# Kernel tuning notes

Measured on AMD Instinct MI355X. Metric: run time of the kernel, lower is better.

## Reference

```python
import jax, jax.numpy as jnp
import numpy as np

N = 10000    # nodes
D = 128      # d_model
K = 16       # d_state
S = 5        # seq_len (tokens per node)
E = 320000   # edges
R = 200      # num relation types
P = E // (S - 1)  # edges sampled per tokenizer step
EPS = 1e-5


def setup_inputs() -> dict:
    key = jax.random.key(0)
    ks = jax.random.split(key, 16)
    sc = 1.0 / np.sqrt(D)
    return {
        "x": jax.random.normal(ks[0], (N, D), jnp.float32),
        "edge_index": jax.random.randint(ks[1], (2, E), 0, N),
        "edge_type": jax.random.randint(ks[2], (E,), 0, R),
        "perms": jax.random.randint(ks[3], (S - 1, P), 0, E),
        "rel_table": jax.random.normal(ks[4], (R, D), jnp.float32) * 0.1,
        "log_A": jax.random.normal(ks[5], (D, K), jnp.float32) * 0.1,
        "W_B": jax.random.normal(ks[6], (D, K), jnp.float32) * sc,
        "W_C": jax.random.normal(ks[7], (D, K), jnp.float32) * sc,
        "W_delta": jax.random.normal(ks[8], (D, D), jnp.float32) * sc,
        "b_delta": jnp.zeros((D,), jnp.float32),
        "W_g": jax.random.normal(ks[9], (D, D), jnp.float32) * sc,
        "b_g": jnp.zeros((D,), jnp.float32),
        "W_out": jax.random.normal(ks[10], (D, D), jnp.float32) * sc,
        "b_out": jnp.zeros((D,), jnp.float32),
        "ln_g": jnp.ones((D,), jnp.float32),
        "ln_b": jnp.zeros((D,), jnp.float32),
    }


def _tokenize(x, edge_index, edge_type, perms, rel_table):
    # x: [N,D]; perms: [S-1,P] -> tokens [N,S,D]
    src, dst = edge_index[0], edge_index[1]
    step_src = src[perms]                    # [S-1,P]
    step_dst = dst[perms]                    # [S-1,P]
    msg = x[step_src] + rel_table[edge_type[perms]]  # [S-1,P,D]
    seg = jax.vmap(lambda i, m: jax.ops.segment_sum(m, i, num_segments=N))(step_dst, msg)  # [S-1,N,D]
    deg = jax.vmap(lambda i: jax.ops.segment_sum(jnp.ones((P,), x.dtype), i, num_segments=N))(step_dst)  # [S-1,N]
    neigh = seg / jnp.clip(deg, 1.0)[..., None]
    return jnp.concatenate([x[:, None, :], jnp.moveaxis(neigh, 0, 1)], axis=1)  # [N,S,D]


def _selective_scan(tokens, log_A, W_B, W_C, W_delta, b_delta):
    # tokens: [N,S,D] -> [N,S,D]
    deltas = jax.nn.softplus(tokens @ W_delta + b_delta)  # [N,S,D]
    Bs = tokens @ W_B                                     # [N,S,K]
    Cs = tokens @ W_C                                     # [N,S,K]
    A_cont = -jnp.exp(log_A)                              # [D,K]
    A_disc = jnp.exp(deltas[..., None] * A_cont)          # [N,S,D,K]
    Bx = deltas[..., None] * Bs[:, :, None, :] * tokens[..., None]  # [N,S,D,K] = B_disc * x_k

    def step(state, xs):
        a, bx, c = xs                          # [N,D,K],[N,D,K],[N,K]
        state = a * state + bx
        y = jnp.einsum('ndk,nk->nd', state, c)
        return state, y

    init = jnp.zeros((tokens.shape[0], D, K), tokens.dtype)
    _, ys = jax.lax.scan(step, init, (jnp.moveaxis(A_disc, 1, 0),
                                      jnp.moveaxis(Bx, 1, 0),
                                      jnp.moveaxis(Cs, 1, 0)))
    return jnp.moveaxis(ys, 0, 1)  # [N,S,D]


def reference(x, edge_index, edge_type, perms, rel_table, log_A, W_B, W_C,
              W_delta, b_delta, W_g, b_g, W_out, b_out, ln_g, ln_b):
    tokens = _tokenize(x, edge_index, edge_type, perms, rel_table)
    out_f = _selective_scan(tokens, log_A, W_B, W_C, W_delta, b_delta)
    out_b = _selective_scan(tokens[:, ::-1, :], log_A, W_B, W_C, W_delta, b_delta)
    scan_out = (out_f + out_b[:, ::-1, :]).mean(axis=1)  # [N,D]
    gate = jax.nn.silu(x @ W_g + b_g)
    res = x + gate * (scan_out @ W_out + b_out)
    mu = res.mean(axis=-1, keepdims=True)
    var = res.var(axis=-1, keepdims=True)
    return (res - mu) / jnp.sqrt(var + EPS) * ln_g + ln_b
```

## Files before the change

### kernel.cpp

```cpp
#include <hip/hip_runtime.h>
#include <hip/hip_bf16.h>
#include <math.h>

#define N_NODES 10000
#define D_MODEL 128
#define E_EDGES 320000
#define P_EDGES 80000
#define LN_EPS 1e-5f
#define CAP 32
#define M_ROWS 50000
#define NCOLS 160

typedef __attribute__((ext_vector_type(8))) short bf16x8;
typedef __attribute__((ext_vector_type(4))) float f32x4;

__device__ __forceinline__ unsigned short f2bf(float f) {
    __hip_bfloat16 h = __float2bfloat16(f);
    return *reinterpret_cast<unsigned short*>(&h);
}
__device__ __forceinline__ float bf2f(unsigned int u) {
    return __uint_as_float(u << 16);
}

__global__ __launch_bounds__(256) void prep_all(
    const float* __restrict__ Wd, const float* __restrict__ Wb,
    const float* __restrict__ Wc, const float* __restrict__ Wg,
    const float* __restrict__ W_out,
    const float* __restrict__ x, const float* __restrict__ rel,
    const int* __restrict__ edge_index, const int* __restrict__ edge_type,
    unsigned short* __restrict__ Bp, unsigned short* __restrict__ Wop,
    unsigned short* __restrict__ Wgp,
    unsigned short* __restrict__ x_bf, unsigned short* __restrict__ rel_bf,
    int* __restrict__ cnt, int4* __restrict__ ed4,
    unsigned short* __restrict__ tokens)
{
    int gid = blockIdx.x * 256 + threadIdx.x;
    if (gid < 20480) {
        int k = gid / NCOLS, n = gid - (gid / NCOLS) * NCOLS;
        float v;
        if (n < 128)      v = Wd[k * 128 + n];
        else if (n < 144) v = Wb[k * 16 + (n - 128)];
        else              v = Wc[k * 16 + (n - 144)];
        Bp[((size_t)(k >> 3) * NCOLS + n) * 8 + (k & 7)] = f2bf(v);
    } else if (gid < 36864) {
        int i = gid - 20480;
        int k = i >> 7, n = i & 127;
        Wop[((size_t)(k >> 3) * 128 + n) * 8 + (k & 7)] = f2bf(W_out[k * 128 + n]);
    } else if (gid < 53248) {
        int i = gid - 36864;
        int k = i >> 7, n = i & 127;
        Wgp[((size_t)(k >> 3) * 128 + n) * 8 + (k & 7)] = f2bf(Wg[k * 128 + n]);
    } else if (gid < 94208) {
        cnt[gid - 53248] = 0;
    } else if (gid < 119808) {
        int i = gid - 94208;
        rel_bf[i] = f2bf(rel[i]);
    } else if (gid < 1399808) {
        int i = gid - 119808;
        unsigned short v = f2bf(x[i]);
        x_bf[i] = v;
        tokens[(size_t)(i >> 7) * 640 + (i & 127)] = v;
    } else if (gid < 1719808) {
        int e = gid - 1399808;
        ed4[e] = make_int4(edge_index[e], edge_index[E_EDGES + e], edge_type[e], 0);
    }
}

__global__ __launch_bounds__(256) void csr_build(
    const int4* __restrict__ ed4, const int* __restrict__ perms,
    int* __restrict__ cnt, int2* __restrict__ slots)
{
    int gid = blockIdx.x * blockDim.x + threadIdx.x;
    if (gid >= 4 * P_EDGES) return;
    int s = gid / P_EDGES;
    int e = perms[gid];
    int4 ed = ed4[e];
    int b = ed.y * 4 + s;
    int pos = atomicAdd(&cnt[b], 1);
    if (pos < CAP) slots[(size_t)b * CAP + pos] = make_int2(ed.x, ed.z);
}

__global__ __launch_bounds__(256) void gather_tokens(
    const unsigned short* __restrict__ x_bf,
    const int* __restrict__ cnt, const int2* __restrict__ slots,
    const unsigned short* __restrict__ rel_bf,
    unsigned short* __restrict__ tokens)
{
    int n = blockIdx.x;
    int w = threadIdx.x >> 6, lane = threadIdx.x & 63;
    int b = n * 4 + w;
    int c = cnt[b];
    int cc = c < CAP ? c : CAP;
    const int2* sl = slots + (size_t)b * CAP;
    const unsigned int* xu = (const unsigned int*)x_bf;
    const unsigned int* ru = (const unsigned int*)rel_bf;
    float ax = 0.f, ay = 0.f;
    int j = 0;
    for (; j + 4 <= cc; j += 4) {
        int4 e01 = *(const int4*)(sl + j);
        int4 e23 = *(const int4*)(sl + j + 2);
        unsigned int x0 = xu[(size_t)e01.x * 64 + lane];
        unsigned int r0 = ru[(size_t)e01.y * 64 + lane];
        unsigned int x1 = xu[(size_t)e01.z * 64 + lane];
        unsigned int r1 = ru[(size_t)e01.w * 64 + lane];
        unsigned int x2 = xu[(size_t)e23.x * 64 + lane];
        unsigned int r2 = ru[(size_t)e23.y * 64 + lane];
        unsigned int x3 = xu[(size_t)e23.z * 64 + lane];
        unsigned int r3 = ru[(size_t)e23.w * 64 + lane];
        ax += (bf2f(x0 & 0xffffu) + bf2f(r0 & 0xffffu))
            + (bf2f(x1 & 0xffffu) + bf2f(r1 & 0xffffu))
            + (bf2f(x2 & 0xffffu) + bf2f(r2 & 0xffffu))
            + (bf2f(x3 & 0xffffu) + bf2f(r3 & 0xffffu));
        ay += (bf2f(x0 >> 16) + bf2f(r0 >> 16))
            + (bf2f(x1 >> 16) + bf2f(r1 >> 16))
            + (bf2f(x2 >> 16) + bf2f(r2 >> 16))
            + (bf2f(x3 >> 16) + bf2f(r3 >> 16));
    }
    if (j + 2 <= cc) {
        int4 e01 = *(const int4*)(sl + j);
        unsigned int x0 = xu[(size_t)e01.x * 64 + lane];
        unsigned int r0 = ru[(size_t)e01.y * 64 + lane];
        unsigned int x1 = xu[(size_t)e01.z * 64 + lane];
        unsigned int r1 = ru[(size_t)e01.w * 64 + lane];
        ax += (bf2f(x0 & 0xffffu) + bf2f(r0 & 0xffffu))
            + (bf2f(x1 & 0xffffu) + bf2f(r1 & 0xffffu));
        ay += (bf2f(x0 >> 16) + bf2f(r0 >> 16))
            + (bf2f(x1 >> 16) + bf2f(r1 >> 16));
        j += 2;
    }
    if (j < cc) {
        int2 se = sl[j];
        unsigned int xa = xu[(size_t)se.x * 64 + lane];
        unsigned int ra = ru[(size_t)se.y * 64 + lane];
        ax += bf2f(xa & 0xffffu) + bf2f(ra & 0xffffu);
        ay += bf2f(xa >> 16) + bf2f(ra >> 16);
    }
    float inv = 1.f / fmaxf((float)c, 1.f);
    unsigned int pack = (unsigned int)f2bf(ax * inv)
                      | ((unsigned int)f2bf(ay * inv) << 16);
    ((unsigned int*)tokens)[((size_t)n * 5 + w + 1) * 64 + lane] = pack;
}

__global__ __launch_bounds__(256, 2) void mega(
    const unsigned short* __restrict__ tokens,
    const unsigned short* __restrict__ Bp,
    const unsigned short* __restrict__ Wop,
    const unsigned short* __restrict__ Wgp,
    const unsigned short* __restrict__ x_bf,
    const float* __restrict__ x,
    const float* __restrict__ log_A,
    const float* __restrict__ b_delta, const float* __restrict__ b_g,
    const float* __restrict__ b_out,
    const float* __restrict__ ln_g, const float* __restrict__ ln_b,
    float* __restrict__ out)
{
    const int tid = threadIdx.x;
    const int wv = tid >> 6, lane = tid & 63;
    const int quad = lane >> 4, l16 = lane & 15;
    const int m0 = blockIdx.x * 80;
    const int n0 = blockIdx.x * 16;

    __shared__ __align__(16) char smem[34816];
    unsigned short* s_delta = (unsigned short*)smem;
    float*          s_bcf   = (float*)(smem + 20480);
    unsigned short* s_so    = (unsigned short*)(smem + 30720);
    float* s_res  = (float*)smem;
    float* s_pmu  = (float*)(smem + 20480);
    float* s_pv2  = (float*)(smem + 21504);
    float* s_mu   = (float*)(smem + 22528);
    float* s_rstd = (float*)(smem + 22592);

    for (int u = wv; u < 50; u += 4) {
        int f = u / 10, t = u - (u / 10) * 10;
        f32x4 acc = {0.f, 0.f, 0.f, 0.f};
        const unsigned short* arow =
            tokens + (size_t)(m0 + f * 16 + l16) * 128 + quad * 8;
        #pragma unroll
        for (int kc = 0; kc < 128; kc += 32) {
            bf16x8 a = *(const bf16x8*)(arow + kc);
            bf16x8 b = *(const bf16x8*)(Bp +
                ((size_t)(kc / 8 + quad) * NCOLS + 16 * t + l16) * 8);
            acc = __builtin_amdgcn_mfma_f32_16x16x32_bf16(a, b, acc, 0, 0, 0);
        }
        int rbase = f * 16 + quad * 4;
        int c = 16 * t + l16;
        #pragma unroll
        for (int reg = 0; reg < 4; ++reg) {
            int r = rbase + reg;
            float v = acc[reg];
            if (t < 8) {
                float z = v + b_delta[c];
                float d = (z > 15.f) ? z : log1pf(__expf(z));
                s_delta[r * 128 + c] = f2bf(d);
            } else {
                s_bcf[r * 32 + (c - 128)] = v;
            }
        }
    }
    __syncthreads();

    {
        const int dim = tid & 127;
        float Ac[16];
        {
            const float4* la = (const float4*)(log_A + dim * 16);
            #pragma unroll
            for (int q = 0; q < 4; ++q) {
                float4 lv = la[q];
                Ac[q * 4 + 0] = -__expf(lv.x);
                Ac[q * 4 + 1] = -__expf(lv.y);
                Ac[q * 4 + 2] = -__expf(lv.z);
                Ac[q * 4 + 3] = -__expf(lv.w);
            }
        }
        #pragma unroll 1
        for (int i = 0; i < 8; ++i) {
            int node = (tid >> 7) + 2 * i;
            const float* bcn = s_bcf + node * 160;
            float tv[5], dl[5];
            {
                const unsigned short* tb =
                    tokens + ((size_t)(n0 + node) * 5) * 128 + dim;
                const unsigned short* db = s_delta + node * 640 + dim;
                #pragma unroll
                for (int s = 0; s < 5; ++s) {
                    tv[s] = bf2f(tb[s * 128]);
                    dl[s] = bf2f(db[s * 128]);
                }
            }
            float st[16], V[16];
            #pragma unroll
            for (int k = 0; k < 16; ++k) { st[k] = 0.f; V[k] = bcn[16 + k]; }
            float total = 0.f;
            #pragma unroll
            for (int s = 0; s < 5; ++s) {
                float dtv = dl[s] * tv[s];
                float yf = 0.f, ub = 0.f;
                #pragma unroll
                for (int k = 0; k < 16; ++k) {
                    float B = bcn[s * 32 + k];
                    float C = bcn[s * 32 + 16 + k];
                    float A = __expf(dl[s] * Ac[k]);
                    st[k] = fmaf(A, st[k], dtv * B);
                    yf = fmaf(st[k], C, yf);
                    ub = fmaf(V[k], B, ub);
                    if (s < 4) V[k] = fmaf(A, V[k], bcn[(s + 1) * 32 + 16 + k]);
                }
                total += yf + dtv * ub;
            }
            s_so[node * 128 + (((dim >> 3) ^ (node & 7)) << 3) + (dim & 7)] =
                f2bf(total * 0.2f);
        }
    }
    __syncthreads();

    {
        f32x4 accO[2] = {{0,0,0,0},{0,0,0,0}};
        f32x4 accG[2] = {{0,0,0,0},{0,0,0,0}};
        const unsigned short* grow = x_bf + (size_t)(n0 + l16) * 128 + quad * 8;
        #pragma unroll
        for (int kc = 0; kc < 128; kc += 32) {
            bf16x8 a = *(const bf16x8*)(s_so + l16 * 128 +
                           (((kc / 8 + quad) ^ (l16 & 7)) << 3));
            bf16x8 ag = *(const bf16x8*)(grow + kc);
            #pragma unroll
            for (int tt = 0; tt < 2; ++tt) {
                int t = wv * 2 + tt;
                size_t bi = ((size_t)(kc / 8 + quad) * 128 + 16 * t + l16) * 8;
                bf16x8 bo = *(const bf16x8*)(Wop + bi);
                bf16x8 bg = *(const bf16x8*)(Wgp + bi);
                accO[tt] = __builtin_amdgcn_mfma_f32_16x16x32_bf16(a,  bo, accO[tt], 0, 0, 0);
                accG[tt] = __builtin_amdgcn_mfma_f32_16x16x32_bf16(ag, bg, accG[tt], 0, 0, 0);
            }
        }

        #pragma unroll
        for (int tt = 0; tt < 2; ++tt) {
            int c = wv * 32 + tt * 16 + l16;
            #pragma unroll
            for (int reg = 0; reg < 4; ++reg) {
                int lrow = quad * 4 + reg;
                float o  = accO[tt][reg] + b_out[c];
                float gl = accG[tt][reg] + b_g[c];
                float gate = gl / (1.f + __expf(-gl));
                s_res[lrow * 132 + c] = x[(size_t)(n0 + lrow) * 128 + c] + gate * o;
            }
        }
        __syncthreads();

        {
            int row = tid >> 4, q = tid & 15;
            float s = 0.f, s2 = 0.f;
            #pragma unroll
            for (int i = 0; i < 8; ++i) {
                float vv = s_res[row * 132 + q + 16 * i];
                s += vv; s2 += vv * vv;
            }
            s_pmu[row * 16 + q] = s; s_pv2[row * 16 + q] = s2;
        }
        __syncthreads();
        if (tid < 16) {
            float s = 0.f, s2 = 0.f;
            #pragma unroll
            for (int i = 0; i < 16; ++i) { s += s_pmu[tid * 16 + i]; s2 += s_pv2[tid * 16 + i]; }
            float mu = s * (1.f / 128.f);
            float var = s2 * (1.f / 128.f) - mu * mu;
            s_mu[tid] = mu;
            s_rstd[tid] = rsqrtf(var + LN_EPS);
        }
        __syncthreads();
        #pragma unroll
        for (int i = 0; i < 8; ++i) {
            int idx = i * 256 + tid;
            int row = idx >> 7, c = idx & 127;
            out[(size_t)(n0 + row) * 128 + c] =
                (s_res[row * 132 + c] - s_mu[row]) * s_rstd[row] * ln_g[c] + ln_b[c];
        }
    }
}

extern "C" void kernel_launch(void* const* d_in, const int* in_sizes, int n_in,
                              void* d_out, int out_size, void* d_ws, size_t ws_size,
                              hipStream_t stream) {
    const float* x          = (const float*)d_in[0];
    const int*   edge_index = (const int*)  d_in[1];
    const int*   edge_type  = (const int*)  d_in[2];
    const int*   perms      = (const int*)  d_in[3];
    const float* rel_table  = (const float*)d_in[4];
    const float* log_A      = (const float*)d_in[5];
    const float* W_B        = (const float*)d_in[6];
    const float* W_C        = (const float*)d_in[7];
    const float* W_delta    = (const float*)d_in[8];
    const float* b_delta    = (const float*)d_in[9];
    const float* W_g        = (const float*)d_in[10];
    const float* b_g        = (const float*)d_in[11];
    const float* W_out      = (const float*)d_in[12];
    const float* b_out      = (const float*)d_in[13];
    const float* ln_g       = (const float*)d_in[14];
    const float* ln_b       = (const float*)d_in[15];

    char* ws = (char*)d_ws;
    int*            cnt    = (int*)           (ws + 0);
    unsigned short* Bp     = (unsigned short*)(ws + 163840);
    unsigned short* Wop    = (unsigned short*)(ws + 204800);
    unsigned short* Wgp    = (unsigned short*)(ws + 237568);
    unsigned short* x_bf   = (unsigned short*)(ws + 270336);
    unsigned short* rel_bf = (unsigned short*)(ws + 2830336);
    int4*           ed4    = (int4*)          (ws + 2881536);
    unsigned short* tokens = (unsigned short*)(ws + 8001536);
    int2*           slots  = (int2*)          (ws + 20801536);

    prep_all<<<6718, 256, 0, stream>>>(
        W_delta, W_B, W_C, W_g, W_out, x, rel_table, edge_index, edge_type,
        Bp, Wop, Wgp, x_bf, rel_bf, cnt, ed4, tokens);

    csr_build<<<(4 * P_EDGES + 255) / 256, 256, 0, stream>>>(
        ed4, perms, cnt, slots);

    gather_tokens<<<N_NODES, 256, 0, stream>>>(
        x_bf, cnt, slots, rel_bf, tokens);

    mega<<<N_NODES / 16, 256, 0, stream>>>(
        tokens, Bp, Wop, Wgp, x_bf, x, log_A, b_delta, b_g, b_out,
        ln_g, ln_b, (float*)d_out);
}
```

Baseline: 219.0 us.

## Fuse CSR build into prep kernel and widen mega kernel to 512 threads

Drops the separate csr_build kernel and the int4 edge repack. Edges are now read directly from edge_index and edge_type inside prep_all, and the slot atomics run there too, with cnt cleared by a hipMemsetAsync beforehand. This saves one launch and one intermediate buffer write and read. The mega kernel now runs 512 threads per block with 8 waves, each wave handling one 16-column tile in the output GEMMs and half as many nodes in the scan, which is meant to raise parallelism per block. The fused path assumes the memset finishes before the atomics, which stream ordering guarantees, and it adds more register pressure under launch_bounds(512,4).

```diff
diff --git a/kernel.cpp b/kernel.cpp
--- a/kernel.cpp
+++ b/kernel.cpp
@@ -28,10 +28,11 @@
     const float* __restrict__ W_out,
     const float* __restrict__ x, const float* __restrict__ rel,
     const int* __restrict__ edge_index, const int* __restrict__ edge_type,
+    const int* __restrict__ perms,
     unsigned short* __restrict__ Bp, unsigned short* __restrict__ Wop,
     unsigned short* __restrict__ Wgp,
     unsigned short* __restrict__ x_bf, unsigned short* __restrict__ rel_bf,
-    int* __restrict__ cnt, int4* __restrict__ ed4,
+    int* __restrict__ cnt, int2* __restrict__ slots,
     unsigned short* __restrict__ tokens)
 {
     int gid = blockIdx.x * 256 + threadIdx.x;
@@ -50,34 +51,25 @@
         int i = gid - 36864;
         int k = i >> 7, n = i & 127;
         Wgp[((size_t)(k >> 3) * 128 + n) * 8 + (k & 7)] = f2bf(Wg[k * 128 + n]);
-    } else if (gid < 94208) {
-        cnt[gid - 53248] = 0;
-    } else if (gid < 119808) {
-        int i = gid - 94208;
+    } else if (gid < 78848) {
+        int i = gid - 53248;
         rel_bf[i] = f2bf(rel[i]);
-    } else if (gid < 1399808) {
-        int i = gid - 119808;
+    } else if (gid < 1358848) {
+        int i = gid - 78848;
         unsigned short v = f2bf(x[i]);
         x_bf[i] = v;
         tokens[(size_t)(i >> 7) * 640 + (i & 127)] = v;
-    } else if (gid < 1719808) {
-        int e = gid - 1399808;
-        ed4[e] = make_int4(edge_index[e], edge_index[E_EDGES + e], edge_type[e], 0);
-    }
-}
-
-__global__ __launch_bounds__(256) void csr_build(
-    const int4* __restrict__ ed4, const int* __restrict__ perms,
-    int* __restrict__ cnt, int2* __restrict__ slots)
-{
-    int gid = blockIdx.x * blockDim.x + threadIdx.x;
-    if (gid >= 4 * P_EDGES) return;
-    int s = gid / P_EDGES;
-    int e = perms[gid];
-    int4 ed = ed4[e];
-    int b = ed.y * 4 + s;
-    int pos = atomicAdd(&cnt[b], 1);
-    if (pos < CAP) slots[(size_t)b * CAP + pos] = make_int2(ed.x, ed.z);
+    } else if (gid < 1678848) {
+        int i = gid - 1358848;
+        int s = i / P_EDGES;
+        int e = perms[i];
+        int src = edge_index[e];
+        int dst = edge_index[E_EDGES + e];
+        int ty  = edge_type[e];
+        int b = dst * 4 + s;
+        int pos = atomicAdd(&cnt[b], 1);
+        if (pos < CAP) slots[(size_t)b * CAP + pos] = make_int2(src, ty);
+    }
 }
 
 __global__ __launch_bounds__(256) void gather_tokens(
@@ -141,7 +133,7 @@
     ((unsigned int*)tokens)[((size_t)n * 5 + w + 1) * 64 + lane] = pack;
 }
 
-__global__ __launch_bounds__(256, 2) void mega(
+__global__ __launch_bounds__(512, 4) void mega(
     const unsigned short* __restrict__ tokens,
     const unsigned short* __restrict__ Bp,
     const unsigned short* __restrict__ Wop,
@@ -170,7 +162,7 @@
     float* s_mu   = (float*)(smem + 22528);
     float* s_rstd = (float*)(smem + 22592);
 
-    for (int u = wv; u < 50; u += 4) {
+    for (int u = wv; u < 50; u += 8) {
         int f = u / 10, t = u - (u / 10) * 10;
         f32x4 acc = {0.f, 0.f, 0.f, 0.f};
         const unsigned short* arow =
@@ -214,8 +206,8 @@
             }
         }
         #pragma unroll 1
-        for (int i = 0; i < 8; ++i) {
-            int node = (tid >> 7) + 2 * i;
+        for (int i = 0; i < 4; ++i) {
+            int node = (tid >> 7) + 4 * i;
             const float* bcn = s_bcf + node * 160;
             float tv[5], dl[5];
             {
@@ -255,40 +247,35 @@
     __syncthreads();
 
     {
-        f32x4 accO[2] = {{0,0,0,0},{0,0,0,0}};
-        f32x4 accG[2] = {{0,0,0,0},{0,0,0,0}};
+        f32x4 accO = {0,0,0,0};
+        f32x4 accG = {0,0,0,0};
         const unsigned short* grow = x_bf + (size_t)(n0 + l16) * 128 + quad * 8;
         #pragma unroll
         for (int kc = 0; kc < 128; kc += 32) {
             bf16x8 a = *(const bf16x8*)(s_so + l16 * 128 +
                            (((kc / 8 + quad) ^ (l16 & 7)) << 3));
             bf16x8 ag = *(const bf16x8*)(grow + kc);
-            #pragma unroll
-            for (int tt = 0; tt < 2; ++tt) {
-                int t = wv * 2 + tt;
-                size_t bi = ((size_t)(kc / 8 + quad) * 128 + 16 * t + l16) * 8;
-                bf16x8 bo = *(const bf16x8*)(Wop + bi);
-                bf16x8 bg = *(const bf16x8*)(Wgp + bi);
-                accO[tt] = __builtin_amdgcn_mfma_f32_16x16x32_bf16(a,  bo, accO[tt], 0, 0, 0);
-                accG[tt] = __builtin_amdgcn_mfma_f32_16x16x32_bf16(ag, bg, accG[tt], 0, 0, 0);
-            }
-        }
-
-        #pragma unroll
-        for (int tt = 0; tt < 2; ++tt) {
-            int c = wv * 32 + tt * 16 + l16;
+            size_t bi = ((size_t)(kc / 8 + quad) * 128 + 16 * wv + l16) * 8;
+            bf16x8 bo = *(const bf16x8*)(Wop + bi);
+            bf16x8 bg = *(const bf16x8*)(Wgp + bi);
+            accO = __builtin_amdgcn_mfma_f32_16x16x32_bf16(a,  bo, accO, 0, 0, 0);
+            accG = __builtin_amdgcn_mfma_f32_16x16x32_bf16(ag, bg, accG, 0, 0, 0);
+        }
+
+        {
+            int c = wv * 16 + l16;
             #pragma unroll
             for (int reg = 0; reg < 4; ++reg) {
                 int lrow = quad * 4 + reg;
-                float o  = accO[tt][reg] + b_out[c];
-                float gl = accG[tt][reg] + b_g[c];
+                float o  = accO[reg] + b_out[c];
+                float gl = accG[reg] + b_g[c];
                 float gate = gl / (1.f + __expf(-gl));
                 s_res[lrow * 132 + c] = x[(size_t)(n0 + lrow) * 128 + c] + gate * o;
             }
         }
         __syncthreads();
 
-        {
+        if (tid < 256) {
             int row = tid >> 4, q = tid & 15;
             float s = 0.f, s2 = 0.f;
             #pragma unroll
@@ -310,8 +297,8 @@
         }
         __syncthreads();
         #pragma unroll
-        for (int i = 0; i < 8; ++i) {
-            int idx = i * 256 + tid;
+        for (int i = 0; i < 4; ++i) {
+            int idx = i * 512 + tid;
             int row = idx >> 7, c = idx & 127;
             out[(size_t)(n0 + row) * 128 + c] =
                 (s_res[row * 132 + c] - s_mu[row]) * s_rstd[row] * ln_g[c] + ln_b[c];
@@ -346,21 +333,19 @@
     unsigned short* Wgp    = (unsigned short*)(ws + 237568);
     unsigned short* x_bf   = (unsigned short*)(ws + 270336);
     unsigned short* rel_bf = (unsigned short*)(ws + 2830336);
-    int4*           ed4    = (int4*)          (ws + 2881536);
-    unsigned short* tokens = (unsigned short*)(ws + 8001536);
-    int2*           slots  = (int2*)          (ws + 20801536);
-
-    prep_all<<<6718, 256, 0, stream>>>(
+    unsigned short* tokens = (unsigned short*)(ws + 2881536);
+    int2*           slots  = (int2*)          (ws + 15681536);
+
+    (void)hipMemsetAsync(cnt, 0, 163840, stream);
+
+    prep_all<<<6558, 256, 0, stream>>>(
         W_delta, W_B, W_C, W_g, W_out, x, rel_table, edge_index, edge_type,
-        Bp, Wop, Wgp, x_bf, rel_bf, cnt, ed4, tokens);
-
-    csr_build<<<(4 * P_EDGES + 255) / 256, 256, 0, stream>>>(
-        ed4, perms, cnt, slots);
+        perms, Bp, Wop, Wgp, x_bf, rel_bf, cnt, slots, tokens);
 
     gather_tokens<<<N_NODES, 256, 0, stream>>>(
         x_bf, cnt, slots, rel_bf, tokens);
 
-    mega<<<N_NODES / 16, 256, 0, stream>>>(
+    mega<<<N_NODES / 16, 512, 0, stream>>>(
         tokens, Bp, Wop, Wgp, x_bf, x, log_A, b_delta, b_g, b_out,
         ln_g, ln_b, (float*)d_out);
 }
```

Result: slower. 342.0 us (+56.2%).
